# Optimization experiments

Measured on AMD Instinct MI355X. Metric: run time of the kernel, lower is better.

The kernel has to match this reference:

```python
import jax, jax.numpy as jnp
import numpy as np

B = 2
L = 512                         # latent dim
NF = [64, 128, 256, 512, 512]   # _get_num_features(2*base_features=64, 64, max=512)


def _rn(key, shape, scale=1.0):
    return scale * jax.random.normal(key, shape, dtype=jnp.float32)


def _blur_up(x):
    """upfirdn2d: 2x upsample + FIR blur with resample_kernel [1,3,3,1], gain=factor**2."""
    k = jnp.array([1.0, 3.0, 3.0, 1.0], dtype=x.dtype)
    kk = jnp.outer(k, k)
    kk = kk / kk.sum() * 4.0  # gain = 2**2
    c = x.shape[-1]
    kern = jnp.broadcast_to(kk[:, :, None, None], (4, 4, 1, c))
    return jax.lax.conv_general_dilated(
        x, kern, (1, 1), ((2, 2), (2, 2)), lhs_dilation=(2, 2),
        dimension_numbers=('NHWC', 'HWIO', 'NHWC'), feature_group_count=c)


def _mod_conv(x, latent, w, b, sw, sb, demodulate):
    """StyleGAN2 modulated conv. x:(B,H,W,Cin), w:(kh,kw,Cin,Cout), style affine (L,Cin)."""
    s = latent @ sw + sb                             # (B,Cin) style
    ww = w[None] * s[:, None, None, :, None]         # (B,kh,kw,Cin,Cout)
    if demodulate:
        d = jax.lax.rsqrt(jnp.sum(ww * ww, axis=(1, 2, 3)) + 1e-8)  # (B,Cout)
        ww = ww * d[:, None, None, None, :]
    def per_sample(xi, wi):
        return jax.lax.conv_general_dilated(
            xi[None], wi, (1, 1), 'SAME',
            dimension_numbers=('NHWC', 'HWIO', 'NHWC'))[0]
    return jax.vmap(per_sample)(x, ww) + b


def _forward(latents, const, w0, b0, sw0, sb0, ns0, noise0, wr0, br0, swr0, sbr0,
             wu1, bu1, swu1, sbu1, wc1, bc1, swc1, sbc1, wr1, br1, swr1, sbr1,
             wu2, bu2, swu2, sbu2, wc2, bc2, swc2, sbc2, wr2, br2, swr2, sbr2,
             wu3, bu3, swu3, sbu3, wc3, bc3, swc3, sbc3, wr3, br3, swr3, sbr3,
             wu4, bu4, swu4, sbu4, wc4, bc4, swc4, sbc4, wr4, br4, swr4, sbr4):
    act = lambda t: jax.nn.leaky_relu(t, 0.01)
    b = latents.shape[0]
    lat = latents.reshape(b, 2, 5, latents.shape[-1])  # (B,2,n_levels,L)
    # first layer at 4x4: modulated conv + noise + leaky_relu (only layer with noise, per source)
    y = _mod_conv(jnp.tile(const[None], (b, 1, 1, 1)), lat[:, 0, 0], w0, b0, sw0, sb0, True)
    y = act(y + ns0 * noise0)
    rgb = act(_mod_conv(y, lat[:, 0, 1], wr0, br0, swr0, sbr0, False))
    ups = [(wu1, bu1, swu1, sbu1), (wu2, bu2, swu2, sbu2), (wu3, bu3, swu3, sbu3), (wu4, bu4, swu4, sbu4)]
    cvs = [(wc1, bc1, swc1, sbc1), (wc2, bc2, swc2, sbc2), (wc3, bc3, swc3, sbc3), (wc4, bc4, swc4, sbc4)]
    rgbs = [(wr1, br1, swr1, sbr1), (wr2, br2, swr2, sbr2), (wr3, br3, swr3, sbr3), (wr4, br4, swr4, sbr4)]
    for i in range(1, 5):
        wu, bu, swu, sbu = ups[i - 1]
        wc, bc, swc, sbc = cvs[i - 1]
        wr, br, swr, sbr = rgbs[i - 1]
        y = _mod_conv(_blur_up(y), lat[:, i - 1, 1], wu, bu, swu, sbu, True)
        # plain ModulatedConv2D 3x3 (no noise/activation in the source loop)
        y = _mod_conv(y, lat[:, i, 0], wc, bc, swc, sbc, True)
        # to_rgb (no demod) + skip accumulation of FIR-upsampled previous rgb
        rgb = act(_mod_conv(y, lat[:, i, 1], wr, br, swr, sbr, False)) + _blur_up(rgb)
    return rgb  # (B,64,64,3)


reference = _forward


def setup_inputs():
    key = jax.random.key(0)
    ks = iter(jax.random.split(key, 80))
    inp = {}
    inp['latents'] = _rn(next(ks), (B, 2 * 5, L))
    inp['const'] = _rn(next(ks), (4, 4, NF[-1]))
    def mod(pfx, kh, cin, cout):
        inp['w' + pfx] = _rn(next(ks), (kh, kh, cin, cout), (kh * kh * cin) ** -0.5)
        inp['b' + pfx] = jnp.zeros((cout,), jnp.float32)
        inp['sw' + pfx] = _rn(next(ks), (L, cin), L ** -0.5)
        inp['sb' + pfx] = jnp.ones((cin,), jnp.float32)
    mod('0', 3, NF[-1], NF[-1])
    inp['ns0'] = 0.1 * _rn(next(ks), (1, 1, 1, 1))
    inp['noise0'] = _rn(next(ks), (B, 4, 4, 1))
    mod('r0', 1, NF[-1], 3)
    cprev = NF[-1]
    for i in range(1, 5):
        c = NF[i]
        mod('u%d' % i, 3, cprev, c)
        mod('c%d' % i, 3, c, c)
        mod('r%d' % i, 1, c, 3)
        cprev = c
    return inp
```

## Files before the change

kernel.cpp:

```cpp
#include <hip/hip_runtime.h>

#define LEAKY(v) ((v) > 0.f ? (v) : 0.01f * (v))

typedef __attribute__((ext_vector_type(8))) short bf16x8;
typedef __attribute__((ext_vector_type(4))) float floatx4;

__device__ inline unsigned short f2bf(float f) {
  unsigned u = __float_as_uint(f);
  unsigned r = u + 0x7FFFu + ((u >> 16) & 1u);
  return (unsigned short)(r >> 16);
}

struct StyleDesc { const float* sw; const float* sb; int row; int cin; };
struct StyleArgs { StyleDesc d[14]; };

__global__ __launch_bounds__(256) void style_all_kernel(
    const float* __restrict__ lat, StyleArgs A, float* __restrict__ S)
{
  int bid = blockIdx.x;
  int chunk = bid & 1, b = (bid >> 1) & 1, sid = bid >> 2;
  StyleDesc d = A.d[sid];
  int ci = chunk * 256 + threadIdx.x;
  if (ci >= d.cin) return;
  const float* l = lat + (size_t)b * (10 * 512) + d.row * 512;
  float a0 = 0.f, a1 = 0.f, a2 = 0.f, a3 = 0.f, a4 = 0.f, a5 = 0.f, a6 = 0.f, a7 = 0.f;
  const float* wp = d.sw + ci;
  size_t st = d.cin;
  for (int k = 0; k < 512; k += 8) {
    a0 += l[k] * wp[0];
    a1 += l[k + 1] * wp[st];
    a2 += l[k + 2] * wp[2 * st];
    a3 += l[k + 3] * wp[3 * st];
    a4 += l[k + 4] * wp[4 * st];
    a5 += l[k + 5] * wp[5 * st];
    a6 += l[k + 6] * wp[6 * st];
    a7 += l[k + 7] * wp[7 * st];
    wp += 8 * st;
  }
  S[sid * 1024 + b * 512 + ci] = d.sb[ci] + ((a0 + a1) + (a2 + a3)) + ((a4 + a5) + (a6 + a7));
}

struct W2D { const float* w; int cinLog; int coutLog; int start; int w2off; };
struct W2Args { W2D d[9]; int total4; };

__global__ __launch_bounds__(256) void w2_kernel(W2Args A, float* __restrict__ W2)
{
  int idx = blockIdx.x * 256 + threadIdx.x;
  if (idx >= A.total4) return;
  int c = 0;
  while (c < 8 && idx >= A.d[c + 1].start) c++;
  W2D d = A.d[c];
  int rel = idx - d.start;
  int co4Log = d.coutLog - 2;
  int ci = rel >> co4Log;
  int co = (rel & ((1 << co4Log) - 1)) << 2;
  size_t ktStride = (size_t)(1 << d.cinLog) << d.coutLog;
  const float* p = d.w + ((size_t)ci << d.coutLog) + co;
  float4 acc = {0.f, 0.f, 0.f, 0.f};
#pragma unroll
  for (int kt = 0; kt < 9; kt++) {
    float4 v = *(const float4*)(p + kt * ktStride);
    acc.x += v.x * v.x; acc.y += v.y * v.y; acc.z += v.z * v.z; acc.w += v.w * v.w;
  }
  *(float4*)(W2 + d.w2off + ((size_t)ci << d.coutLog) + co) = acc;
}

struct D2D { int w2off; int sid; int did; int cin; int cout; int start; };
struct D2Args { D2D d[9]; };

__global__ __launch_bounds__(256) void demod2_all_kernel(
    D2Args A, const float* __restrict__ W2, const float* __restrict__ S,
    float* __restrict__ Dout)
{
  __shared__ float red[256];
  int bid = blockIdx.x;
  int c = 0;
  while (c < 8 && bid >= A.d[c + 1].start) c++;
  D2D d = A.d[c];
  int rel = bid - d.start;
  int chunksPerB = d.cout >> 6;
  int b = rel / chunksPerB;
  int coc = rel - b * chunksPerB;
  int co = coc * 64 + (threadIdx.x & 63);
  int slice = threadIdx.x >> 6;
  const float* sv = S + d.sid * 1024 + b * 512;
  const float* wp = W2 + d.w2off + co;
  float a0 = 0.f, a1 = 0.f, a2 = 0.f, a3 = 0.f, a4 = 0.f, a5 = 0.f, a6 = 0.f, a7 = 0.f;
  for (int r = slice; r < d.cin; r += 32) {
    float s0 = sv[r];          a0 += s0 * s0 * wp[(size_t)r * d.cout];
    float s1 = sv[r + 4];      a1 += s1 * s1 * wp[(size_t)(r + 4) * d.cout];
    float s2 = sv[r + 8];      a2 += s2 * s2 * wp[(size_t)(r + 8) * d.cout];
    float s3 = sv[r + 12];     a3 += s3 * s3 * wp[(size_t)(r + 12) * d.cout];
    float s4 = sv[r + 16];     a4 += s4 * s4 * wp[(size_t)(r + 16) * d.cout];
    float s5 = sv[r + 20];     a5 += s5 * s5 * wp[(size_t)(r + 20) * d.cout];
    float s6 = sv[r + 24];     a6 += s6 * s6 * wp[(size_t)(r + 24) * d.cout];
    float s7 = sv[r + 28];     a7 += s7 * s7 * wp[(size_t)(r + 28) * d.cout];
  }
  red[threadIdx.x] = ((a0 + a1) + (a2 + a3)) + ((a4 + a5) + (a6 + a7));
  __syncthreads();
  if (threadIdx.x < 64) {
    float a = red[threadIdx.x] + red[threadIdx.x + 64] + red[threadIdx.x + 128] + red[threadIdx.x + 192];
    Dout[d.did * 1024 + b * 512 + co] = rsqrtf(a + 1e-8f);
  }
}

struct WPD { const float* src; unsigned short* dst; int cin; int cout; int start; };
struct WPArgs { WPD d[6]; int total; };

__global__ __launch_bounds__(256) void wprep_kernel(WPArgs A)
{
  int chunk = blockIdx.x * 256 + threadIdx.x;
  if (chunk >= A.total) return;
  int c = 0;
  while (c < 5 && chunk >= A.d[c + 1].start) c++;
  WPD d = A.d[c];
  int rel = chunk - d.start;
  int cpc = d.cin * 9 / 8;
  int co = rel / cpc;
  int k0 = (rel - co * cpc) * 8;
  int cig = k0 / 288;
  int r = k0 - cig * 288;
  int kt = r >> 5;
  int cibase = cig * 32 + (r & 31);
  const float* sp = d.src + (size_t)(kt * d.cin + cibase) * d.cout + co;
  size_t st = d.cout;
  unsigned r0 = f2bf(sp[0]) | ((unsigned)f2bf(sp[st]) << 16);
  unsigned r1 = f2bf(sp[2 * st]) | ((unsigned)f2bf(sp[3 * st]) << 16);
  unsigned r2 = f2bf(sp[4 * st]) | ((unsigned)f2bf(sp[5 * st]) << 16);
  unsigned r3 = f2bf(sp[6 * st]) | ((unsigned)f2bf(sp[7 * st]) << 16);
  uint4 v = {r0, r1, r2, r3};
  *(uint4*)(d.dst + (size_t)co * (d.cin * 9) + k0) = v;
}

__device__ inline void blur_taps(int o, int* r0, int* r1, float* w0, float* w1)
{
  if ((o & 1) == 0) { *r0 = (o >> 1) - 1; *w0 = 1.f; *r1 = (o >> 1); *w1 = 3.f; }
  else              { *r0 = (o - 1) >> 1; *w0 = 3.f; *r1 = ((o - 1) >> 1) + 1; *w1 = 1.f; }
}

__global__ __launch_bounds__(256) void blur_up_kernel(
    const float* __restrict__ x, int H, int W, int C, float* __restrict__ out)
{
  int b = blockIdx.y;
  int W2 = W * 2;
  int pix = blockIdx.x;
  int oy = pix / W2, ox = pix % W2;
  int ry0, ry1, rx0, rx1; float wy0, wy1, wx0, wx1;
  blur_taps(oy, &ry0, &ry1, &wy0, &wy1);
  blur_taps(ox, &rx0, &rx1, &wx0, &wx1);
  bool vy0 = (ry0 >= 0 && ry0 < H), vy1 = (ry1 >= 0 && ry1 < H);
  bool vx0 = (rx0 >= 0 && rx0 < W), vx1 = (rx1 >= 0 && rx1 < W);
  const float* base = x + (size_t)b * H * W * C;
  float* ob = out + (((size_t)b * W2 + oy) * W2 + ox) * C;
  for (int c = threadIdx.x; c < C; c += 256) {
    float acc = 0.f;
    if (vy0) {
      const float* r = base + (size_t)(ry0 * W) * C;
      if (vx0) acc += wy0 * wx0 * r[(size_t)rx0 * C + c];
      if (vx1) acc += wy0 * wx1 * r[(size_t)rx1 * C + c];
    }
    if (vy1) {
      const float* r = base + (size_t)(ry1 * W) * C;
      if (vx0) acc += wy1 * wx0 * r[(size_t)rx0 * C + c];
      if (vx1) acc += wy1 * wx1 * r[(size_t)rx1 * C + c];
    }
    ob[c] = acc * (1.f / 16.f);
  }
}

__global__ __launch_bounds__(256) void prep_up_kernel(
    const float* __restrict__ y, int Hc, int C,
    const float* __restrict__ s, unsigned short* __restrict__ out)
{
  int b = blockIdx.y;
  int W2 = Hc * 2;
  int pix = blockIdx.x;
  int oy = pix / W2, ox = pix - oy * W2;
  int ry0, ry1, rx0, rx1; float wy0, wy1, wx0, wx1;
  blur_taps(oy, &ry0, &ry1, &wy0, &wy1);
  blur_taps(ox, &rx0, &rx1, &wx0, &wx1);
  bool vy0 = (ry0 >= 0 && ry0 < Hc), vy1 = (ry1 >= 0 && ry1 < Hc);
  bool vx0 = (rx0 >= 0 && rx0 < Hc), vx1 = (rx1 >= 0 && rx1 < Hc);
  const float* base = y + (size_t)b * Hc * Hc * C;
  unsigned short* ob = out + (((size_t)b * W2 + oy) * W2 + ox) * C;
  const float* sv = s + b * 512;
  for (int c = threadIdx.x; c < C; c += 256) {
    float acc = 0.f;
    if (vy0) {
      const float* r = base + (size_t)(ry0 * Hc) * C;
      if (vx0) acc += wy0 * wx0 * r[(size_t)rx0 * C + c];
      if (vx1) acc += wy0 * wx1 * r[(size_t)rx1 * C + c];
    }
    if (vy1) {
      const float* r = base + (size_t)(ry1 * Hc) * C;
      if (vx0) acc += wy1 * wx0 * r[(size_t)rx0 * C + c];
      if (vx1) acc += wy1 * wx1 * r[(size_t)rx1 * C + c];
    }
    ob[c] = f2bf(acc * (1.f / 16.f) * sv[c]);
  }
}

__global__ __launch_bounds__(256) void mfma_conv_kernel(
    const unsigned short* __restrict__ xp, int H, int WLOG, int Cin, int Cout,
    const unsigned short* __restrict__ wT,
    const float* __restrict__ bias, const float* __restrict__ dmod,
    float* __restrict__ outF, unsigned short* __restrict__ outBf,
    const float* __restrict__ sNext)
{
  extern __shared__ unsigned short sm[];
  const int W = 1 << WLOG;
  const int Rt = 128 >> WLOG;
  const int PR = Rt + 2, PC = W + 2;
  const int patchU = PR * PC * 40;
  unsigned short* Bw = sm + patchU;

  const int tid = threadIdx.x;
  const int wave = tid >> 6;
  const int lane = tid & 63;
  const int q = lane >> 4;
  const int l15 = lane & 15;

  const int HW = H << WLOG;
  const int m0 = blockIdx.x << 7;
  const int b = m0 / HW;
  const int y0 = (m0 - b * HW) >> WLOG;
  const int co0 = blockIdx.y << 6;
  const int Kp = Cin * 9;
  const unsigned short* xb = xp + (size_t)b * HW * Cin;

  const int pSlots = PR * PC * 4;
  int pLds[5], pSrc[5];
#pragma unroll
  for (int i = 0; i < 5; i++) {
    int sidx = tid + i * 256;
    pLds[i] = -1; pSrc[i] = -1;
    if (sidx < pSlots) {
      int pidx = sidx >> 2, part = sidx & 3;
      int pr = pidx / PC, pc = pidx - pr * PC;
      int gy = y0 + pr - 1, gx = pc - 1;
      pLds[i] = pidx * 40 + part * 8;
      if ((unsigned)gy < (unsigned)H && (unsigned)gx < (unsigned)W)
        pSrc[i] = ((gy << WLOG) + gx) * Cin + part * 8;
    }
  }
  int bLds[9], bSrc[9];
#pragma unroll
  for (int i = 0; i < 9; i++) {
    int sidx = tid + i * 256;
    int n = sidx / 36, c16 = sidx - n * 36;
    bLds[i] = n * 296 + c16 * 8;
    bSrc[i] = (co0 + n) * Kp + c16 * 8;
  }

  floatx4 zero = {0.f, 0.f, 0.f, 0.f};
  floatx4 acc[2][4];
#pragma unroll
  for (int mi = 0; mi < 2; mi++)
#pragma unroll
    for (int s = 0; s < 4; s++) acc[mi][s] = zero;

  const int mA0 = wave * 32 + l15;
  const int mA1 = mA0 + 16;
  const int aBase0 = ((mA0 >> WLOG) * PC + (mA0 & (W - 1))) * 40 + q * 8;
  const int aBase1 = ((mA1 >> WLOG) * PC + (mA1 & (W - 1))) * 40 + q * 8;
  const int bBase = l15 * 296 + q * 8;

  const int nGroups = Cin >> 5;
  for (int g = 0; g < nGroups; g++) {
    __syncthreads();
    {
      const int gci = g << 5;
#pragma unroll
      for (int i = 0; i < 5; i++) {
        if (pLds[i] >= 0) {
          uint4 v = {0u, 0u, 0u, 0u};
          if (pSrc[i] >= 0) v = *(const uint4*)(xb + pSrc[i] + gci);
          *(uint4*)(sm + pLds[i]) = v;
        }
      }
      const int gw = g * 288;
#pragma unroll
      for (int i = 0; i < 9; i++)
        *(uint4*)(Bw + bLds[i]) = *(const uint4*)(wT + bSrc[i] + gw);
    }
    __syncthreads();
#pragma unroll
    for (int kt = 0; kt < 9; kt++) {
      const int ky = kt / 3, kx = kt - (kt / 3) * 3;
      const int ao = (ky * PC + kx) * 40;
      bf16x8 a0 = *(const bf16x8*)(sm + aBase0 + ao);
      bf16x8 a1 = *(const bf16x8*)(sm + aBase1 + ao);
      const int bo = bBase + kt * 32;
#pragma unroll
      for (int s = 0; s < 4; s++) {
        bf16x8 bb = *(const bf16x8*)(Bw + bo + s * (16 * 296));
        acc[0][s] = __builtin_amdgcn_mfma_f32_16x16x32_bf16(a0, bb, acc[0][s], 0, 0, 0);
        acc[1][s] = __builtin_amdgcn_mfma_f32_16x16x32_bf16(a1, bb, acc[1][s], 0, 0, 0);
      }
    }
  }

#pragma unroll
  for (int s = 0; s < 4; s++) {
    const int co = co0 + s * 16 + l15;
    const float dm = dmod[b * 512 + co];
    const float bv = bias[co];
    const float sn = sNext ? sNext[b * 512 + co] : 0.f;
#pragma unroll
    for (int mi = 0; mi < 2; mi++) {
#pragma unroll
      for (int r = 0; r < 4; r++) {
        const int mloc = wave * 32 + mi * 16 + q * 4 + r;
        const int py = y0 + (mloc >> WLOG);
        const int px = mloc & (W - 1);
        const size_t oidx = (((size_t)b * H + py) * W + px) * Cout + co;
        const float v = acc[mi][s][r] * dm + bv;
        if (outF) outF[oidx] = v;
        if (outBf) outBf[oidx] = f2bf(v * sn);
      }
    }
  }
}

template<int PIX, int NCI4>
__global__ __launch_bounds__(256) void modconv_splitk_kernel(
    const float* __restrict__ x, size_t xBStride, int H, int W, int cinShift,
    int Cout,
    const float* __restrict__ w, const float* __restrict__ s,
    float* __restrict__ partial)
{
  constexpr int NCI = NCI4 * 4;
  constexpr int CLOG = (NCI == 16) ? 4 : (NCI == 32) ? 5 : 6;
  extern __shared__ float lds[];
  const int COLS = PIX + 2;
  const int tid = threadIdx.x;
  const int nthr = blockDim.x;
  const int b = blockIdx.y;
  const int z = blockIdx.z;
  const int ci0 = z << CLOG;
  const int wb = W / PIX;
  const int row = blockIdx.x / wb;
  const int x0 = (blockIdx.x % wb) * PIX;

  const float* xb = x + (size_t)b * xBStride;
  const float* sv = s + b * 512;

  const int tot = 3 * COLS << CLOG;
  for (int idx = tid; idx < tot; idx += nthr) {
    int cil = idx & (NCI - 1);
    int t = idx >> CLOG;
    int col = t % COLS;
    int ry = t / COLS;
    int gy = row + ry - 1;
    int gx = x0 + col - 1;
    float v = 0.f;
    if (gy >= 0 && gy < H && gx >= 0 && gx < W)
      v = xb[((size_t)(gy * W + gx) << cinShift) + ci0 + cil] * sv[ci0 + cil];
    lds[idx] = v;
  }
  __syncthreads();

  float acc0[PIX];
  float acc1[PIX];
#pragma unroll
  for (int p = 0; p < PIX; p++) { acc0[p] = 0.f; acc1[p] = 0.f; }
  const int co0 = tid;
  const int co1 = tid + nthr;
  const bool a0 = co0 < Cout;
  const bool a1 = co1 < Cout;
  const int d01 = nthr;

  const float4* ldsv = (const float4*)lds;
  constexpr int cin4Shift = CLOG - 2;

  for (int kt = 0; kt < 9; kt++) {
    int ky = kt / 3, kx = kt % 3;
    const float* wr = w + ((size_t)(kt << cinShift) + ci0) * Cout + co0;
#pragma unroll
    for (int c4 = 0; c4 < NCI4; c4++) {
      float wA0 = 0.f, wA1 = 0.f, wA2 = 0.f, wA3 = 0.f;
      float wB0 = 0.f, wB1 = 0.f, wB2 = 0.f, wB3 = 0.f;
      const float* wq = wr + (size_t)c4 * 4 * Cout;
      if (a0) { wA0 = wq[0]; }
      if (a1) { wB0 = wq[d01]; }
      if (a0) { wA1 = wq[Cout]; }
      if (a1) { wB1 = wq[Cout + d01]; }
      if (a0) { wA2 = wq[2 * Cout]; }
      if (a1) { wB2 = wq[2 * Cout + d01]; }
      if (a0) { wA3 = wq[3 * Cout]; }
      if (a1) { wB3 = wq[3 * Cout + d01]; }
#pragma unroll
      for (int p = 0; p < PIX; p++) {
        float4 v = ldsv[((ky * COLS + kx + p) << cin4Shift) + c4];
        acc0[p] += v.x * wA0; acc0[p] += v.y * wA1; acc0[p] += v.z * wA2; acc0[p] += v.w * wA3;
        acc1[p] += v.x * wB0; acc1[p] += v.y * wB1; acc1[p] += v.z * wB2; acc1[p] += v.w * wB3;
      }
    }
  }

  const int HW = H * W;
  float* pb = partial + ((size_t)(z * gridDim.y + b) * HW + row * W + x0) * Cout;
#pragma unroll
  for (int p = 0; p < PIX; p++) {
    if (a0) pb[(size_t)p * Cout + co0] = acc0[p];
    if (a1) pb[(size_t)p * Cout + co1] = acc1[p];
  }
}

__global__ __launch_bounds__(256) void splitk_epi_kernel(
    const float* __restrict__ partial, int nz, int M, int Cout, int HW,
    const float* __restrict__ dmod, const float* __restrict__ bias,
    const float* __restrict__ noise, const float* __restrict__ ns,
    float* __restrict__ out, int doAct)
{
  int idx = blockIdx.x * 256 + threadIdx.x;
  if (idx >= M * Cout) return;
  int m = idx / Cout;
  int co = idx - m * Cout;
  int b = m / HW;
  float acc = 0.f;
  for (int z = 0; z < nz; z++) acc += partial[(size_t)z * M * Cout + idx];
  float v = acc * dmod[b * 512 + co] + bias[co];
  if (noise) v += ns[0] * noise[m];
  if (doAct) v = LEAKY(v);
  out[idx] = v;
}

__global__ __launch_bounds__(64) void rgb_kernel(
    const float* __restrict__ y, int H, int W, int Cin,
    const float* __restrict__ w, const float* __restrict__ bias,
    const float* __restrict__ s, const float* __restrict__ prev,
    float* __restrict__ out)
{
  int b = blockIdx.y;
  int pix = blockIdx.x;
  int oy = pix / W, ox = pix % W;
  const float* xp = y + (((size_t)b * H + oy) * W + ox) * Cin;
  const float* sv = s + b * 512;
  float p0 = 0.f, p1 = 0.f, p2 = 0.f;
  for (int ci = threadIdx.x; ci < Cin; ci += 64) {
    float v = xp[ci] * sv[ci];
    p0 += v * w[ci * 3 + 0];
    p1 += v * w[ci * 3 + 1];
    p2 += v * w[ci * 3 + 2];
  }
  for (int off = 32; off > 0; off >>= 1) {
    p0 += __shfl_down(p0, off);
    p1 += __shfl_down(p1, off);
    p2 += __shfl_down(p2, off);
  }
  if (threadIdx.x == 0) {
    float r0 = p0 + bias[0], r1 = p1 + bias[1], r2 = p2 + bias[2];
    float sk0 = 0.f, sk1 = 0.f, sk2 = 0.f;
    if (prev) {
      int Hp = H >> 1, Wp = W >> 1;
      int ry0, ry1, rx0, rx1; float wy0, wy1, wx0, wx1;
      blur_taps(oy, &ry0, &ry1, &wy0, &wy1);
      blur_taps(ox, &rx0, &rx1, &wx0, &wx1);
      bool vy0 = (ry0 >= 0 && ry0 < Hp), vy1 = (ry1 >= 0 && ry1 < Hp);
      bool vx0 = (rx0 >= 0 && rx0 < Wp), vx1 = (rx1 >= 0 && rx1 < Wp);
      const float* base = prev + (size_t)b * Hp * Wp * 3;
      float a0 = 0.f, a1 = 0.f, a2 = 0.f;
      if (vy0 && vx0) { const float* qq = base + (size_t)(ry0 * Wp + rx0) * 3; float wg = wy0 * wx0; a0 += wg * qq[0]; a1 += wg * qq[1]; a2 += wg * qq[2]; }
      if (vy0 && vx1) { const float* qq = base + (size_t)(ry0 * Wp + rx1) * 3; float wg = wy0 * wx1; a0 += wg * qq[0]; a1 += wg * qq[1]; a2 += wg * qq[2]; }
      if (vy1 && vx0) { const float* qq = base + (size_t)(ry1 * Wp + rx0) * 3; float wg = wy1 * wx0; a0 += wg * qq[0]; a1 += wg * qq[1]; a2 += wg * qq[2]; }
      if (vy1 && vx1) { const float* qq = base + (size_t)(ry1 * Wp + rx1) * 3; float wg = wy1 * wx1; a0 += wg * qq[0]; a1 += wg * qq[1]; a2 += wg * qq[2]; }
      sk0 = a0 * (1.f / 16.f); sk1 = a1 * (1.f / 16.f); sk2 = a2 * (1.f / 16.f);
    }
    float* ob = out + (((size_t)b * H + oy) * W + ox) * 3;
    ob[0] = LEAKY(r0) + sk0;
    ob[1] = LEAKY(r1) + sk1;
    ob[2] = LEAKY(r2) + sk2;
  }
}

extern "C" void kernel_launch(void* const* d_in, const int* in_sizes, int n_in,
                              void* d_out, int out_size, void* d_ws, size_t ws_size,
                              hipStream_t stream)
{
  auto F = [&](int k) { return (const float*)d_in[k]; };
  const float* latents = F(0);
  const float* cnst = F(1);
  const float* w0 = F(2);  const float* b0 = F(3);  const float* sw0 = F(4);  const float* sb0 = F(5);
  const float* ns0 = F(6); const float* noise0 = F(7);
  const float* wr0 = F(8); const float* br0 = F(9); const float* swr0 = F(10); const float* sbr0 = F(11);
  const float *wu[4], *bu[4], *swu[4], *sbu[4];
  const float *wc[4], *bc[4], *swc[4], *sbc[4];
  const float *wr[4], *br_[4], *swr[4], *sbr[4];
  int k = 12;
  for (int l = 0; l < 4; l++) {
    wu[l] = F(k++); bu[l] = F(k++); swu[l] = F(k++); sbu[l] = F(k++);
    wc[l] = F(k++); bc[l] = F(k++); swc[l] = F(k++); sbc[l] = F(k++);
    wr[l] = F(k++); br_[l] = F(k++); swr[l] = F(k++); sbr[l] = F(k++);
  }

  float* ws = (float*)d_ws;
  float* S = ws;
  float* D = S + 14 * 1024;
  float* W2 = D + 9 * 1024;
  float* bufA = W2 + 1359872;
  float* bufB = bufA + 2 * 64 * 64 * 512;
  float* rgbA = bufB + 2 * 64 * 64 * 512;
  float* rgbB = rgbA + 2 * 64 * 64 * 3;
  float* P = rgbB + 2 * 64 * 64 * 3;
  unsigned short* u16 = (unsigned short*)(P + 262144);
  unsigned short* xprepA = u16;
  unsigned short* xprepB = xprepA + 2 * 64 * 64 * 512;
  unsigned short* wT[6];
  {
    unsigned short* p = xprepB + 2 * 64 * 64 * 512;
    int wsz[6] = {9 * 128 * 256, 9 * 256 * 256, 9 * 256 * 512, 9 * 512 * 512, 9 * 512 * 512, 9 * 512 * 512};
    for (int i = 0; i < 6; i++) { wT[i] = p; p += wsz[i]; }
  }

  const int B = 2;
  const int NFa[5] = {64, 128, 256, 512, 512};
  int cprev0[4] = {512, 128, 256, 512};
  int rowu[4] = {1, 6, 6, 6};

  const float* cw[9]  = {w0, wu[0], wc[0], wu[1], wc[1], wu[2], wc[2], wu[3], wc[3]};
  int cinL[9]  = {9, 9, 7, 7, 8, 8, 9, 9, 9};
  int coutL[9] = {9, 7, 7, 8, 8, 9, 9, 9, 9};
  int sidOf[9] = {0, 2, 3, 5, 6, 8, 9, 11, 12};
  int didOf[9] = {0, 1, 2, 3, 4, 5, 6, 7, 8};

  {
    WPArgs WA;
    const float* srcs[6] = {wu[1], wc[1], wu[2], wc[2], wu[3], wc[3]};
    int cins[6] = {128, 256, 256, 512, 512, 512};
    int couts[6] = {256, 256, 512, 512, 512, 512};
    int start = 0;
    for (int i = 0; i < 6; i++) {
      WA.d[i] = {srcs[i], wT[i], cins[i], couts[i], start};
      start += couts[i] * cins[i] * 9 / 8;
    }
    WA.total = start;
    wprep_kernel<<<dim3((start + 255) / 256), 256, 0, stream>>>(WA);
  }

  {
    StyleArgs SA;
    SA.d[0] = {sw0, sb0, 0, 512};
    SA.d[1] = {swr0, sbr0, 1, 512};
    for (int l = 0; l < 4; l++) {
      int c = NFa[l + 1];
      SA.d[2 + l * 3] = {swu[l], sbu[l], rowu[l], cprev0[l]};
      SA.d[3 + l * 3] = {swc[l], sbc[l], 5, c};
      SA.d[4 + l * 3] = {swr[l], sbr[l], 6, c};
    }
    style_all_kernel<<<dim3(56), 256, 0, stream>>>(latents, SA, S);
  }

  int w2off[9];
  {
    W2Args WA2;
    int start = 0, off = 0;
    for (int i = 0; i < 9; i++) {
      w2off[i] = off;
      WA2.d[i] = {cw[i], cinL[i], coutL[i], start, off};
      int elems = 1 << (cinL[i] + coutL[i]);
      start += elems >> 2;
      off += elems;
    }
    WA2.total4 = start;
    w2_kernel<<<dim3((start + 255) / 256), 256, 0, stream>>>(WA2, W2);
  }

  {
    D2Args DA;
    int start = 0;
    for (int i = 0; i < 9; i++) {
      int cout = 1 << coutL[i];
      DA.d[i] = {w2off[i], sidOf[i], didOf[i], 1 << cinL[i], cout, start};
      start += B * (cout >> 6);
    }
    demod2_all_kernel<<<dim3(start), 256, 0, stream>>>(DA, W2, S, D);
  }

  modconv_splitk_kernel<4, 8><<<dim3(4, B, 16), 256, (size_t)3 * 6 * 32 * 4, stream>>>(
      cnst, 0, 4, 4, 9, 512, w0, S, P);
  splitk_epi_kernel<<<dim3((32 * 512 + 255) / 256), 256, 0, stream>>>(
      P, 16, 32, 512, 16, D, b0, noise0, ns0, bufA, 1);
  rgb_kernel<<<dim3(16, B), 64, 0, stream>>>(bufA, 4, 4, 512, wr0, br0, S + 1024, nullptr, rgbA);

  blur_up_kernel<<<dim3(64, B), 256, 0, stream>>>(bufA, 4, 4, 512, bufB);
  modconv_splitk_kernel<8, 8><<<dim3(8, B, 16), 128, (size_t)3 * 10 * 32 * 4, stream>>>(
      bufB, (size_t)64 * 512, 8, 8, 9, 128, wu[0], S + 2 * 1024, P);
  splitk_epi_kernel<<<dim3((128 * 128 + 255) / 256), 256, 0, stream>>>(
      P, 16, 128, 128, 64, D + 1 * 1024, bu[0], nullptr, nullptr, bufA, 0);
  modconv_splitk_kernel<8, 4><<<dim3(8, B, 8), 128, (size_t)3 * 10 * 16 * 4, stream>>>(
      bufA, (size_t)64 * 128, 8, 8, 7, 128, wc[0], S + 3 * 1024, P);
  splitk_epi_kernel<<<dim3((128 * 128 + 255) / 256), 256, 0, stream>>>(
      P, 8, 128, 128, 64, D + 2 * 1024, bc[0], nullptr, nullptr, bufB, 0);
  rgb_kernel<<<dim3(64, B), 64, 0, stream>>>(bufB, 8, 8, 128, wr[0], br_[0], S + 4 * 1024, rgbA, rgbB);

  float* ybuf[4] = {bufB, bufA, bufB, bufA};
  float* rgbp = rgbB;
  const float* ysrc = bufB;
  int Hc = 8;
  for (int l = 1; l < 4; l++) {
    int c = NFa[l + 1];
    int cp = cprev0[l];
    int H2 = Hc * 2;
    int WLOG = (H2 == 16) ? 4 : (H2 == 32) ? 5 : 6;
    int wi = (l - 1) * 2;
    prep_up_kernel<<<dim3(H2 * H2, B), 256, 0, stream>>>(
        ysrc, Hc, cp, S + (2 + l * 3) * 1024, xprepA);
    {
      int PRu = (128 >> WLOG) + 2, PCu = H2 + 2;
      size_t lds = (size_t)(PRu * PCu * 40 + 64 * 296) * 2;
      mfma_conv_kernel<<<dim3((B * H2 * H2) / 128, c >> 6), 256, lds, stream>>>(
          xprepA, H2, WLOG, cp, c, wT[wi], bu[l], D + (1 + l * 2) * 1024,
          nullptr, xprepB, S + (3 + l * 3) * 1024);
    }
    float* yo = ybuf[l];
    {
      int PRu = (128 >> WLOG) + 2, PCu = H2 + 2;
      size_t lds = (size_t)(PRu * PCu * 40 + 64 * 296) * 2;
      mfma_conv_kernel<<<dim3((B * H2 * H2) / 128, c >> 6), 256, lds, stream>>>(
          xprepB, H2, WLOG, c, c, wT[wi + 1], bc[l], D + (2 + l * 2) * 1024,
          yo, nullptr, nullptr);
    }
    float* rout = (l == 3) ? (float*)d_out : ((rgbp == rgbA) ? rgbB : rgbA);
    rgb_kernel<<<dim3(H2 * H2, B), 64, 0, stream>>>(
        yo, H2, H2, c, wr[l], br_[l], S + (4 + l * 3) * 1024, rgbp, rout);
    rgbp = (rout == rgbA) ? rgbA : rgbB;
    ysrc = yo;
    Hc = H2;
  }
  (void)in_sizes; (void)n_in; (void)out_size; (void)ws_size;
}
```

Before: 625.7 us.

## Fuse prep kernels, blur into first upsample conv, epilogue with to_rgb; repad LDS

Merges the style, squared-weight and weight-prep kernels into one launch. Folds the 4x4→8x8 blur-upsample into a new split-K conv kernel and fuses the split-K epilogue with the to_rgb projection and skip blur at low resolutions. Changes the split-K factors and the LDS row padding in the MFMA conv, loading fragments as two 8-byte halves. This cuts launch count and intermediate buffer traffic, but changes bank-conflict behaviour and the size of the partial-sum buffer.

```diff
diff --git a/kernel.cpp b/kernel.cpp
--- a/kernel.cpp
+++ b/kernel.cpp
@@ -3,6 +3,7 @@
 #define LEAKY(v) ((v) > 0.f ? (v) : 0.01f * (v))
 
 typedef __attribute__((ext_vector_type(8))) short bf16x8;
+typedef __attribute__((ext_vector_type(4))) short bf16x4;
 typedef __attribute__((ext_vector_type(4))) float floatx4;
 
 __device__ inline unsigned short f2bf(float f) {
@@ -11,13 +12,22 @@
   return (unsigned short)(r >> 16);
 }
 
+__device__ inline bf16x8 ld_frag8(const unsigned short* p) {
+  bf16x4 lo = *(const bf16x4*)p;
+  bf16x4 hi = *(const bf16x4*)(p + 4);
+  return __builtin_shufflevector(lo, hi, 0, 1, 2, 3, 4, 5, 6, 7);
+}
+
 struct StyleDesc { const float* sw; const float* sb; int row; int cin; };
 struct StyleArgs { StyleDesc d[14]; };
-
-__global__ __launch_bounds__(256) void style_all_kernel(
-    const float* __restrict__ lat, StyleArgs A, float* __restrict__ S)
-{
-  int bid = blockIdx.x;
+struct W2D { const float* w; int cinLog; int coutLog; int start; int w2off; };
+struct W2Args { W2D d[9]; int total4; };
+struct WPD { const float* src; unsigned short* dst; int cin; int cout; int start; };
+struct WPArgs { WPD d[6]; int total; };
+
+__device__ void style_body(int bid, const float* __restrict__ lat, const StyleArgs& A,
+                           float* __restrict__ S)
+{
   int chunk = bid & 1, b = (bid >> 1) & 1, sid = bid >> 2;
   StyleDesc d = A.d[sid];
   int ci = chunk * 256 + threadIdx.x;
@@ -40,12 +50,8 @@
   S[sid * 1024 + b * 512 + ci] = d.sb[ci] + ((a0 + a1) + (a2 + a3)) + ((a4 + a5) + (a6 + a7));
 }
 
-struct W2D { const float* w; int cinLog; int coutLog; int start; int w2off; };
-struct W2Args { W2D d[9]; int total4; };
-
-__global__ __launch_bounds__(256) void w2_kernel(W2Args A, float* __restrict__ W2)
-{
-  int idx = blockIdx.x * 256 + threadIdx.x;
+__device__ void w2_body(int idx, const W2Args& A, float* __restrict__ W2)
+{
   if (idx >= A.total4) return;
   int c = 0;
   while (c < 8 && idx >= A.d[c + 1].start) c++;
@@ -63,6 +69,42 @@
     acc.x += v.x * v.x; acc.y += v.y * v.y; acc.z += v.z * v.z; acc.w += v.w * v.w;
   }
   *(float4*)(W2 + d.w2off + ((size_t)ci << d.coutLog) + co) = acc;
+}
+
+__device__ void wprep_body(int chunk, const WPArgs& A)
+{
+  if (chunk >= A.total) return;
+  int c = 0;
+  while (c < 5 && chunk >= A.d[c + 1].start) c++;
+  WPD d = A.d[c];
+  int rel = chunk - d.start;
+  int cpc = d.cin * 9 / 8;
+  int co = rel / cpc;
+  int k0 = (rel - co * cpc) * 8;
+  int cig = k0 / 288;
+  int r = k0 - cig * 288;
+  int kt = r >> 5;
+  int cibase = cig * 32 + (r & 31);
+  const float* sp = d.src + (size_t)(kt * d.cin + cibase) * d.cout + co;
+  size_t st = d.cout;
+  unsigned r0 = f2bf(sp[0]) | ((unsigned)f2bf(sp[st]) << 16);
+  unsigned r1 = f2bf(sp[2 * st]) | ((unsigned)f2bf(sp[3 * st]) << 16);
+  unsigned r2 = f2bf(sp[4 * st]) | ((unsigned)f2bf(sp[5 * st]) << 16);
+  unsigned r3 = f2bf(sp[6 * st]) | ((unsigned)f2bf(sp[7 * st]) << 16);
+  uint4 v = {r0, r1, r2, r3};
+  *(uint4*)(d.dst + (size_t)co * (d.cin * 9) + k0) = v;
+}
+
+__global__ __launch_bounds__(256) void prep_all_kernel(
+    const float* __restrict__ lat, StyleArgs SA, W2Args WA, WPArgs PA,
+    float* __restrict__ S, float* __restrict__ W2, int styleBlocks, int w2Blocks)
+{
+  int bid = blockIdx.x;
+  if (bid < styleBlocks) { style_body(bid, lat, SA, S); return; }
+  bid -= styleBlocks;
+  if (bid < w2Blocks) { w2_body(bid * 256 + threadIdx.x, WA, W2); return; }
+  bid -= w2Blocks;
+  wprep_body(bid * 256 + threadIdx.x, PA);
 }
 
 struct D2D { int w2off; int sid; int did; int cin; int cout; int start; };
@@ -104,68 +146,10 @@
   }
 }
 
-struct WPD { const float* src; unsigned short* dst; int cin; int cout; int start; };
-struct WPArgs { WPD d[6]; int total; };
-
-__global__ __launch_bounds__(256) void wprep_kernel(WPArgs A)
-{
-  int chunk = blockIdx.x * 256 + threadIdx.x;
-  if (chunk >= A.total) return;
-  int c = 0;
-  while (c < 5 && chunk >= A.d[c + 1].start) c++;
-  WPD d = A.d[c];
-  int rel = chunk - d.start;
-  int cpc = d.cin * 9 / 8;
-  int co = rel / cpc;
-  int k0 = (rel - co * cpc) * 8;
-  int cig = k0 / 288;
-  int r = k0 - cig * 288;
-  int kt = r >> 5;
-  int cibase = cig * 32 + (r & 31);
-  const float* sp = d.src + (size_t)(kt * d.cin + cibase) * d.cout + co;
-  size_t st = d.cout;
-  unsigned r0 = f2bf(sp[0]) | ((unsigned)f2bf(sp[st]) << 16);
-  unsigned r1 = f2bf(sp[2 * st]) | ((unsigned)f2bf(sp[3 * st]) << 16);
-  unsigned r2 = f2bf(sp[4 * st]) | ((unsigned)f2bf(sp[5 * st]) << 16);
-  unsigned r3 = f2bf(sp[6 * st]) | ((unsigned)f2bf(sp[7 * st]) << 16);
-  uint4 v = {r0, r1, r2, r3};
-  *(uint4*)(d.dst + (size_t)co * (d.cin * 9) + k0) = v;
-}
-
 __device__ inline void blur_taps(int o, int* r0, int* r1, float* w0, float* w1)
 {
   if ((o & 1) == 0) { *r0 = (o >> 1) - 1; *w0 = 1.f; *r1 = (o >> 1); *w1 = 3.f; }
   else              { *r0 = (o - 1) >> 1; *w0 = 3.f; *r1 = ((o - 1) >> 1) + 1; *w1 = 1.f; }
-}
-
-__global__ __launch_bounds__(256) void blur_up_kernel(
-    const float* __restrict__ x, int H, int W, int C, float* __restrict__ out)
-{
-  int b = blockIdx.y;
-  int W2 = W * 2;
-  int pix = blockIdx.x;
-  int oy = pix / W2, ox = pix % W2;
-  int ry0, ry1, rx0, rx1; float wy0, wy1, wx0, wx1;
-  blur_taps(oy, &ry0, &ry1, &wy0, &wy1);
-  blur_taps(ox, &rx0, &rx1, &wx0, &wx1);
-  bool vy0 = (ry0 >= 0 && ry0 < H), vy1 = (ry1 >= 0 && ry1 < H);
-  bool vx0 = (rx0 >= 0 && rx0 < W), vx1 = (rx1 >= 0 && rx1 < W);
-  const float* base = x + (size_t)b * H * W * C;
-  float* ob = out + (((size_t)b * W2 + oy) * W2 + ox) * C;
-  for (int c = threadIdx.x; c < C; c += 256) {
-    float acc = 0.f;
-    if (vy0) {
-      const float* r = base + (size_t)(ry0 * W) * C;
-      if (vx0) acc += wy0 * wx0 * r[(size_t)rx0 * C + c];
-      if (vx1) acc += wy0 * wx1 * r[(size_t)rx1 * C + c];
-    }
-    if (vy1) {
-      const float* r = base + (size_t)(ry1 * W) * C;
-      if (vx0) acc += wy1 * wx0 * r[(size_t)rx0 * C + c];
-      if (vx1) acc += wy1 * wx1 * r[(size_t)rx1 * C + c];
-    }
-    ob[c] = acc * (1.f / 16.f);
-  }
 }
 
 __global__ __launch_bounds__(256) void prep_up_kernel(
@@ -211,7 +195,7 @@
   const int W = 1 << WLOG;
   const int Rt = 128 >> WLOG;
   const int PR = Rt + 2, PC = W + 2;
-  const int patchU = PR * PC * 40;
+  const int patchU = PR * PC * 36;
   unsigned short* Bw = sm + patchU;
 
   const int tid = threadIdx.x;
@@ -238,7 +222,7 @@
       int pidx = sidx >> 2, part = sidx & 3;
       int pr = pidx / PC, pc = pidx - pr * PC;
       int gy = y0 + pr - 1, gx = pc - 1;
-      pLds[i] = pidx * 40 + part * 8;
+      pLds[i] = pidx * 36 + part * 8;
       if ((unsigned)gy < (unsigned)H && (unsigned)gx < (unsigned)W)
         pSrc[i] = ((gy << WLOG) + gx) * Cin + part * 8;
     }
@@ -248,7 +232,7 @@
   for (int i = 0; i < 9; i++) {
     int sidx = tid + i * 256;
     int n = sidx / 36, c16 = sidx - n * 36;
-    bLds[i] = n * 296 + c16 * 8;
+    bLds[i] = n * 292 + c16 * 8;
     bSrc[i] = (co0 + n) * Kp + c16 * 8;
   }
 
@@ -261,9 +245,9 @@
 
   const int mA0 = wave * 32 + l15;
   const int mA1 = mA0 + 16;
-  const int aBase0 = ((mA0 >> WLOG) * PC + (mA0 & (W - 1))) * 40 + q * 8;
-  const int aBase1 = ((mA1 >> WLOG) * PC + (mA1 & (W - 1))) * 40 + q * 8;
-  const int bBase = l15 * 296 + q * 8;
+  const int aBase0 = ((mA0 >> WLOG) * PC + (mA0 & (W - 1))) * 36 + q * 8;
+  const int aBase1 = ((mA1 >> WLOG) * PC + (mA1 & (W - 1))) * 36 + q * 8;
+  const int bBase = l15 * 292 + q * 8;
 
   const int nGroups = Cin >> 5;
   for (int g = 0; g < nGroups; g++) {
@@ -275,25 +259,31 @@
         if (pLds[i] >= 0) {
           uint4 v = {0u, 0u, 0u, 0u};
           if (pSrc[i] >= 0) v = *(const uint4*)(xb + pSrc[i] + gci);
-          *(uint4*)(sm + pLds[i]) = v;
+          uint2 lo = {v.x, v.y}, hi = {v.z, v.w};
+          *(uint2*)(sm + pLds[i]) = lo;
+          *(uint2*)(sm + pLds[i] + 4) = hi;
         }
       }
       const int gw = g * 288;
 #pragma unroll
-      for (int i = 0; i < 9; i++)
-        *(uint4*)(Bw + bLds[i]) = *(const uint4*)(wT + bSrc[i] + gw);
+      for (int i = 0; i < 9; i++) {
+        uint4 v = *(const uint4*)(wT + bSrc[i] + gw);
+        uint2 lo = {v.x, v.y}, hi = {v.z, v.w};
+        *(uint2*)(Bw + bLds[i]) = lo;
+        *(uint2*)(Bw + bLds[i] + 4) = hi;
+      }
     }
     __syncthreads();
 #pragma unroll
     for (int kt = 0; kt < 9; kt++) {
       const int ky = kt / 3, kx = kt - (kt / 3) * 3;
-      const int ao = (ky * PC + kx) * 40;
-      bf16x8 a0 = *(const bf16x8*)(sm + aBase0 + ao);
-      bf16x8 a1 = *(const bf16x8*)(sm + aBase1 + ao);
+      const int ao = (ky * PC + kx) * 36;
+      bf16x8 a0 = ld_frag8(sm + aBase0 + ao);
+      bf16x8 a1 = ld_frag8(sm + aBase1 + ao);
       const int bo = bBase + kt * 32;
 #pragma unroll
       for (int s = 0; s < 4; s++) {
-        bf16x8 bb = *(const bf16x8*)(Bw + bo + s * (16 * 296));
+        bf16x8 bb = ld_frag8(Bw + bo + s * (16 * 292));
         acc[0][s] = __builtin_amdgcn_mfma_f32_16x16x32_bf16(a0, bb, acc[0][s], 0, 0, 0);
         acc[1][s] = __builtin_amdgcn_mfma_f32_16x16x32_bf16(a1, bb, acc[1][s], 0, 0, 0);
       }
@@ -407,11 +397,79 @@
   }
 }
 
+__global__ __launch_bounds__(128) void modconv_splitk_blur_kernel(
+    const float* __restrict__ y, const float* __restrict__ w,
+    const float* __restrict__ s, float* __restrict__ partial)
+{
+  extern __shared__ float lds[];
+  const int tid = threadIdx.x;
+  const int b = blockIdx.y;
+  const int z = blockIdx.z;
+  const int ci0 = z << 4;
+  const int row = blockIdx.x;
+
+  const float* yb = y + (size_t)b * 16 * 512;
+  const float* sv = s + b * 512;
+
+  for (int idx = tid; idx < 480; idx += 128) {
+    int cil = idx & 15;
+    int t = idx >> 4;
+    int col = t % 10;
+    int ry = t / 10;
+    int gy = row + ry - 1;
+    int gx = col - 1;
+    float v = 0.f;
+    if ((unsigned)gy < 8u && (unsigned)gx < 8u) {
+      int ry0, ry1, rx0, rx1; float wy0, wy1, wx0, wx1;
+      blur_taps(gy, &ry0, &ry1, &wy0, &wy1);
+      blur_taps(gx, &rx0, &rx1, &wx0, &wx1);
+      bool vy0 = (ry0 >= 0 && ry0 < 4), vy1 = (ry1 >= 0 && ry1 < 4);
+      bool vx0 = (rx0 >= 0 && rx0 < 4), vx1 = (rx1 >= 0 && rx1 < 4);
+      int ci = ci0 + cil;
+      float acc = 0.f;
+      if (vy0 && vx0) acc += wy0 * wx0 * yb[((ry0 * 4 + rx0) << 9) + ci];
+      if (vy0 && vx1) acc += wy0 * wx1 * yb[((ry0 * 4 + rx1) << 9) + ci];
+      if (vy1 && vx0) acc += wy1 * wx0 * yb[((ry1 * 4 + rx0) << 9) + ci];
+      if (vy1 && vx1) acc += wy1 * wx1 * yb[((ry1 * 4 + rx1) << 9) + ci];
+      v = acc * (1.f / 16.f) * sv[ci];
+    }
+    lds[idx] = v;
+  }
+  __syncthreads();
+
+  float acc0[8];
+#pragma unroll
+  for (int p = 0; p < 8; p++) acc0[p] = 0.f;
+  const int co0 = tid;
+  const float4* ldsv = (const float4*)lds;
+
+  for (int kt = 0; kt < 9; kt++) {
+    int ky = kt / 3, kx = kt % 3;
+    const float* wr = w + ((size_t)(kt << 9) + ci0) * 128 + co0;
+#pragma unroll
+    for (int c4 = 0; c4 < 4; c4++) {
+      const float* wq = wr + (size_t)c4 * 4 * 128;
+      float wA0 = wq[0];
+      float wA1 = wq[128];
+      float wA2 = wq[256];
+      float wA3 = wq[384];
+#pragma unroll
+      for (int p = 0; p < 8; p++) {
+        float4 v = ldsv[((ky * 10 + kx + p) << 2) + c4];
+        acc0[p] += v.x * wA0; acc0[p] += v.y * wA1; acc0[p] += v.z * wA2; acc0[p] += v.w * wA3;
+      }
+    }
+  }
+
+  float* pb = partial + ((size_t)(z * gridDim.y + b) * 64 + row * 8) * 128;
+#pragma unroll
+  for (int p = 0; p < 8; p++) pb[(size_t)p * 128 + co0] = acc0[p];
+}
+
 __global__ __launch_bounds__(256) void splitk_epi_kernel(
     const float* __restrict__ partial, int nz, int M, int Cout, int HW,
     const float* __restrict__ dmod, const float* __restrict__ bias,
-    const float* __restrict__ noise, const float* __restrict__ ns,
-    float* __restrict__ out, int doAct)
+    float* __restrict__ out)
 {
   int idx = blockIdx.x * 256 + threadIdx.x;
   if (idx >= M * Cout) return;
@@ -420,10 +478,65 @@
   int b = m / HW;
   float acc = 0.f;
   for (int z = 0; z < nz; z++) acc += partial[(size_t)z * M * Cout + idx];
+  out[idx] = acc * dmod[b * 512 + co] + bias[co];
+}
+
+__global__ void epirgb_kernel(
+    const float* __restrict__ P, int nz, int HW, int Cout, int W,
+    const float* __restrict__ dmod, const float* __restrict__ bias,
+    const float* __restrict__ noise, const float* __restrict__ ns, int doAct,
+    const float* __restrict__ sR, const float* __restrict__ wR, const float* __restrict__ bR,
+    const float* __restrict__ prev,
+    float* __restrict__ yout, float* __restrict__ rgbout)
+{
+  __shared__ float red[24];
+  int b = blockIdx.x / HW;
+  int pix = blockIdx.x - b * HW;
+  int co = threadIdx.x;
+  int m = b * HW + pix;
+  float acc = 0.f;
+  for (int z = 0; z < nz; z++) acc += P[((size_t)(z * 2 + b) * HW + pix) * Cout + co];
   float v = acc * dmod[b * 512 + co] + bias[co];
   if (noise) v += ns[0] * noise[m];
   if (doAct) v = LEAKY(v);
-  out[idx] = v;
+  yout[(size_t)m * Cout + co] = v;
+  float t = v * sR[b * 512 + co];
+  float r0 = t * wR[co * 3 + 0];
+  float r1 = t * wR[co * 3 + 1];
+  float r2 = t * wR[co * 3 + 2];
+  for (int off = 32; off > 0; off >>= 1) {
+    r0 += __shfl_down(r0, off);
+    r1 += __shfl_down(r1, off);
+    r2 += __shfl_down(r2, off);
+  }
+  int wv = threadIdx.x >> 6, lane = threadIdx.x & 63;
+  if (lane == 0) { red[wv * 3 + 0] = r0; red[wv * 3 + 1] = r1; red[wv * 3 + 2] = r2; }
+  __syncthreads();
+  if (threadIdx.x == 0) {
+    int nw = blockDim.x >> 6;
+    float s0 = bR[0], s1 = bR[1], s2 = bR[2];
+    for (int w = 0; w < nw; w++) { s0 += red[w * 3]; s1 += red[w * 3 + 1]; s2 += red[w * 3 + 2]; }
+    s0 = LEAKY(s0); s1 = LEAKY(s1); s2 = LEAKY(s2);
+    if (prev) {
+      int oy = pix / W, ox = pix - (pix / W) * W;
+      int Hp = W >> 1;
+      int ry0, ry1, rx0, rx1; float wy0, wy1, wx0, wx1;
+      blur_taps(oy, &ry0, &ry1, &wy0, &wy1);
+      blur_taps(ox, &rx0, &rx1, &wx0, &wx1);
+      bool vy0 = (ry0 >= 0 && ry0 < Hp), vy1 = (ry1 >= 0 && ry1 < Hp);
+      bool vx0 = (rx0 >= 0 && rx0 < Hp), vx1 = (rx1 >= 0 && rx1 < Hp);
+      const float* base = prev + (size_t)b * Hp * Hp * 3;
+      float a0 = 0.f, a1 = 0.f, a2 = 0.f;
+      if (vy0 && vx0) { const float* qq = base + (size_t)(ry0 * Hp + rx0) * 3; float wg = wy0 * wx0; a0 += wg * qq[0]; a1 += wg * qq[1]; a2 += wg * qq[2]; }
+      if (vy0 && vx1) { const float* qq = base + (size_t)(ry0 * Hp + rx1) * 3; float wg = wy0 * wx1; a0 += wg * qq[0]; a1 += wg * qq[1]; a2 += wg * qq[2]; }
+      if (vy1 && vx0) { const float* qq = base + (size_t)(ry1 * Hp + rx0) * 3; float wg = wy1 * wx0; a0 += wg * qq[0]; a1 += wg * qq[1]; a2 += wg * qq[2]; }
+      if (vy1 && vx1) { const float* qq = base + (size_t)(ry1 * Hp + rx1) * 3; float wg = wy1 * wx1; a0 += wg * qq[0]; a1 += wg * qq[1]; a2 += wg * qq[2]; }
+      s0 += a0 * (1.f / 16.f); s1 += a1 * (1.f / 16.f); s2 += a2 * (1.f / 16.f);
+    }
+    rgbout[(size_t)m * 3 + 0] = s0;
+    rgbout[(size_t)m * 3 + 1] = s1;
+    rgbout[(size_t)m * 3 + 2] = s2;
+  }
 }
 
 __global__ __launch_bounds__(64) void rgb_kernel(
@@ -503,7 +616,7 @@
   float* rgbA = bufB + 2 * 64 * 64 * 512;
   float* rgbB = rgbA + 2 * 64 * 64 * 3;
   float* P = rgbB + 2 * 64 * 64 * 3;
-  unsigned short* u16 = (unsigned short*)(P + 262144);
+  unsigned short* u16 = (unsigned short*)(P + 524288);
   unsigned short* xprepA = u16;
   unsigned short* xprepB = xprepA + 2 * 64 * 64 * 512;
   unsigned short* wT[6];
@@ -524,20 +637,7 @@
   int sidOf[9] = {0, 2, 3, 5, 6, 8, 9, 11, 12};
   int didOf[9] = {0, 1, 2, 3, 4, 5, 6, 7, 8};
 
-  {
-    WPArgs WA;
-    const float* srcs[6] = {wu[1], wc[1], wu[2], wc[2], wu[3], wc[3]};
-    int cins[6] = {128, 256, 256, 512, 512, 512};
-    int couts[6] = {256, 256, 512, 512, 512, 512};
-    int start = 0;
-    for (int i = 0; i < 6; i++) {
-      WA.d[i] = {srcs[i], wT[i], cins[i], couts[i], start};
-      start += couts[i] * cins[i] * 9 / 8;
-    }
-    WA.total = start;
-    wprep_kernel<<<dim3((start + 255) / 256), 256, 0, stream>>>(WA);
-  }
-
+  int w2off[9];
   {
     StyleArgs SA;
     SA.d[0] = {sw0, sb0, 0, 512};
@@ -548,22 +648,33 @@
       SA.d[3 + l * 3] = {swc[l], sbc[l], 5, c};
       SA.d[4 + l * 3] = {swr[l], sbr[l], 6, c};
     }
-    style_all_kernel<<<dim3(56), 256, 0, stream>>>(latents, SA, S);
-  }
-
-  int w2off[9];
-  {
     W2Args WA2;
-    int start = 0, off = 0;
+    int w2start = 0, off = 0;
     for (int i = 0; i < 9; i++) {
       w2off[i] = off;
-      WA2.d[i] = {cw[i], cinL[i], coutL[i], start, off};
+      WA2.d[i] = {cw[i], cinL[i], coutL[i], w2start, off};
       int elems = 1 << (cinL[i] + coutL[i]);
-      start += elems >> 2;
+      w2start += elems >> 2;
       off += elems;
     }
-    WA2.total4 = start;
-    w2_kernel<<<dim3((start + 255) / 256), 256, 0, stream>>>(WA2, W2);
+    WA2.total4 = w2start;
+    WPArgs WPA;
+    {
+      const float* srcs[6] = {wu[1], wc[1], wu[2], wc[2], wu[3], wc[3]};
+      int cins[6] = {128, 256, 256, 512, 512, 512};
+      int couts[6] = {256, 256, 512, 512, 512, 512};
+      int start = 0;
+      for (int i = 0; i < 6; i++) {
+        WPA.d[i] = {srcs[i], wT[i], cins[i], couts[i], start};
+        start += couts[i] * cins[i] * 9 / 8;
+      }
+      WPA.total = start;
+    }
+    int styleBlocks = 56;
+    int w2Blocks = (WA2.total4 + 255) / 256;
+    int wpBlocks = (WPA.total + 255) / 256;
+    prep_all_kernel<<<dim3(styleBlocks + w2Blocks + wpBlocks), 256, 0, stream>>>(
+        latents, SA, WA2, WPA, S, W2, styleBlocks, w2Blocks);
   }
 
   {
@@ -577,22 +688,21 @@
     demod2_all_kernel<<<dim3(start), 256, 0, stream>>>(DA, W2, S, D);
   }
 
-  modconv_splitk_kernel<4, 8><<<dim3(4, B, 16), 256, (size_t)3 * 6 * 32 * 4, stream>>>(
+  modconv_splitk_kernel<4, 4><<<dim3(4, B, 32), 256, (size_t)3 * 6 * 16 * 4, stream>>>(
       cnst, 0, 4, 4, 9, 512, w0, S, P);
-  splitk_epi_kernel<<<dim3((32 * 512 + 255) / 256), 256, 0, stream>>>(
-      P, 16, 32, 512, 16, D, b0, noise0, ns0, bufA, 1);
-  rgb_kernel<<<dim3(16, B), 64, 0, stream>>>(bufA, 4, 4, 512, wr0, br0, S + 1024, nullptr, rgbA);
-
-  blur_up_kernel<<<dim3(64, B), 256, 0, stream>>>(bufA, 4, 4, 512, bufB);
-  modconv_splitk_kernel<8, 8><<<dim3(8, B, 16), 128, (size_t)3 * 10 * 32 * 4, stream>>>(
-      bufB, (size_t)64 * 512, 8, 8, 9, 128, wu[0], S + 2 * 1024, P);
+  epirgb_kernel<<<dim3(B * 16), 512, 0, stream>>>(
+      P, 32, 16, 512, 4, D, b0, noise0, ns0, 1,
+      S + 1024, wr0, br0, nullptr, bufA, rgbA);
+
+  modconv_splitk_blur_kernel<<<dim3(8, B, 32), 128, (size_t)480 * 4, stream>>>(
+      bufA, wu[0], S + 2 * 1024, P);
   splitk_epi_kernel<<<dim3((128 * 128 + 255) / 256), 256, 0, stream>>>(
-      P, 16, 128, 128, 64, D + 1 * 1024, bu[0], nullptr, nullptr, bufA, 0);
+      P, 32, 128, 128, 64, D + 1 * 1024, bu[0], bufA);
   modconv_splitk_kernel<8, 4><<<dim3(8, B, 8), 128, (size_t)3 * 10 * 16 * 4, stream>>>(
       bufA, (size_t)64 * 128, 8, 8, 7, 128, wc[0], S + 3 * 1024, P);
-  splitk_epi_kernel<<<dim3((128 * 128 + 255) / 256), 256, 0, stream>>>(
-      P, 8, 128, 128, 64, D + 2 * 1024, bc[0], nullptr, nullptr, bufB, 0);
-  rgb_kernel<<<dim3(64, B), 64, 0, stream>>>(bufB, 8, 8, 128, wr[0], br_[0], S + 4 * 1024, rgbA, rgbB);
+  epirgb_kernel<<<dim3(B * 64), 128, 0, stream>>>(
+      P, 8, 64, 128, 8, D + 2 * 1024, bc[0], nullptr, nullptr, 0,
+      S + 4 * 1024, wr[0], br_[0], rgbA, bufB, rgbB);
 
   float* ybuf[4] = {bufB, bufA, bufB, bufA};
   float* rgbp = rgbB;
@@ -608,7 +718,7 @@
         ysrc, Hc, cp, S + (2 + l * 3) * 1024, xprepA);
     {
       int PRu = (128 >> WLOG) + 2, PCu = H2 + 2;
-      size_t lds = (size_t)(PRu * PCu * 40 + 64 * 296) * 2;
+      size_t lds = (size_t)(PRu * PCu * 36 + 64 * 292) * 2;
       mfma_conv_kernel<<<dim3((B * H2 * H2) / 128, c >> 6), 256, lds, stream>>>(
           xprepA, H2, WLOG, cp, c, wT[wi], bu[l], D + (1 + l * 2) * 1024,
           nullptr, xprepB, S + (3 + l * 3) * 1024);
@@ -616,7 +726,7 @@
     float* yo = ybuf[l];
     {
       int PRu = (128 >> WLOG) + 2, PCu = H2 + 2;
-      size_t lds = (size_t)(PRu * PCu * 40 + 64 * 296) * 2;
+      size_t lds = (size_t)(PRu * PCu * 36 + 64 * 292) * 2;
       mfma_conv_kernel<<<dim3((B * H2 * H2) / 128, c >> 6), 256, lds, stream>>>(
           xprepB, H2, WLOG, c, c, wT[wi + 1], bc[l], D + (2 + l * 2) * 1024,
           yo, nullptr, nullptr);
```

Result: no change. 629.9 us (+0.7%).
